# Performance work log

Hardware: AMD Instinct MI355X
Metric: run time of the kernel (lower is better)

## Reference

```python
import jax, jax.numpy as jnp
import numpy as np

B, C, D, H, W = 4, 1, 4, 768, 768
STRICT_MAXIMA_BONUS = 10.0

_c = slice(1, -1)
_l = slice(0, -2)
_r = slice(2, None)


def _pad_rep(x):
    # replicate-pad the three spatial dims by 1 (matches F.pad mode='replicate')
    return jnp.pad(x, ((0, 0), (0, 0), (1, 1), (1, 1), (1, 1)), mode='edge')


def _grads(x):
    """kornia spatial_gradient3d(mode='diff') order 1 and 2, incl. the D-axis
    kernel flip kornia applies before conv3d (negates the ys/xs cross terms)."""
    p = _pad_rep(x)
    gx = 0.5 * (p[:, :, _c, _c, _r] - p[:, :, _c, _c, _l])
    gy = 0.5 * (p[:, :, _c, _r, _c] - p[:, :, _c, _l, _c])
    gs = 0.5 * (p[:, :, _r, _c, _c] - p[:, :, _l, _c, _c])
    dxx = p[:, :, _c, _c, _r] - 2.0 * x + p[:, :, _c, _c, _l]
    dyy = p[:, :, _c, _r, _c] - 2.0 * x + p[:, :, _c, _l, _c]
    dss = p[:, :, _r, _c, _c] - 2.0 * x + p[:, :, _l, _c, _c]
    # cross terms, scaled by 0.25 as in conv_quad_interp3d
    dxy = 0.25 * (p[:, :, _c, _r, _r] - p[:, :, _c, _r, _l] - p[:, :, _c, _l, _r] + p[:, :, _c, _l, _l])
    dys = -0.25 * (p[:, :, _r, _r, _c] - p[:, :, _r, _l, _c] - p[:, :, _l, _r, _c] + p[:, :, _l, _l, _c])
    dxs = -0.25 * (p[:, :, _r, _c, _r] - p[:, :, _r, _c, _l] - p[:, :, _l, _c, _r] + p[:, :, _l, _c, _l])
    return gx, gy, gs, dxx, dyy, dss, dxy, dys, dxs


def _nms3d_strict(x):
    """kornia nms3d 3x3x3 mask: x strictly greater than all 26 neighbours
    (replicate padded) AND x > 0 (the zeroed-center kernel channel)."""
    p = _pad_rep(x)
    sl = [_l, _c, _r]
    m = jnp.zeros_like(x)  # center channel of the NMS kernel is zeroed
    for a in range(3):
        for b in range(3):
            for c3 in range(3):
                if a == 1 and b == 1 and c3 == 1:
                    continue
                m = jnp.maximum(m, p[:, :, sl[a], sl[b], sl[c3]])
    return x > m


def _conv_quad_interp3d(x, strict_maxima_bonus):
    gx, gy, gs, dxx, dyy, dss, dxy, dys, dxs = _grads(x)
    nms_mask = _nms3d_strict(x)
    # per-voxel symmetric 3x3 Cramer solve H s = g
    cf00 = dyy * dss - dys * dys
    cf01 = dxy * dss - dys * dxs
    cf02 = dxy * dys - dyy * dxs
    det = dxx * cf00 - dxy * cf01 + dxs * cf02
    solved = jnp.abs(det) > 0.0
    safe_det = jnp.where(solved, det, jnp.ones_like(det))
    r0, r1, r2 = gx, gy, gs
    sx = (r0 * cf00 - dxy * (r1 * dss - dys * r2) + dxs * (r1 * dys - dyy * r2)) / safe_det
    sy = (dxx * (r1 * dss - dys * r2) - r0 * cf01 + dxs * (dxy * r2 - r1 * dxs)) / safe_det
    ss = (dxx * (dyy * r2 - r1 * dys) - dxy * (dxy * r2 - r1 * dxs) + r0 * cf02) / safe_det
    valid = nms_mask & solved
    # x_solved only where NMS & non-singular; dx = -x_solved
    dx_x = jnp.where(valid, -sx, 0.0)
    dx_y = jnp.where(valid, -sy, 0.0)
    dx_s = jnp.where(valid, -ss, 0.0)
    # reject offsets with |component| > 0.7
    big = jnp.maximum(jnp.maximum(jnp.abs(dx_x), jnp.abs(dx_y)), jnp.abs(dx_s)) > 0.7
    dx_x = jnp.where(big, 0.0, dx_x)
    dx_y = jnp.where(big, 0.0, dx_y)
    dx_s = jnp.where(big, 0.0, dx_s)
    # dy = 0.5 * b^T dx
    dy = 0.5 * (gx * dx_x + gy * dx_y + gs * dx_s)
    y_max = x + dy
    if strict_maxima_bonus > 0:
        y_max = y_max + strict_maxima_bonus * valid.astype(x.dtype)
    # coords: channel order (d, x, y) as in kornia create_meshgrid3d + channel swap
    b_, c_, d_, h_, w_ = x.shape
    zz = jnp.arange(d_, dtype=x.dtype).reshape(1, 1, d_, 1, 1)
    xxg = jnp.arange(w_, dtype=x.dtype).reshape(1, 1, 1, 1, w_)
    yyg = jnp.arange(h_, dtype=x.dtype).reshape(1, 1, 1, h_, 1)
    coords_max = jnp.stack([zz + dx_s, xxg + dx_x, yyg + dx_y], axis=2)  # (B,C,3,D,H,W)
    return coords_max, y_max


def setup_inputs() -> dict:
    key = jax.random.key(0)
    x = jax.random.normal(key, (B, C, D, H, W), dtype=jnp.float32)
    return {"x": x}


def reference(x):
    return _conv_quad_interp3d(x, STRICT_MAXIMA_BONUS)
```

## Files before the change

### kernel.cpp

```cpp
#include <hip/hip_runtime.h>

namespace {
constexpr int Bn = 4, Dn = 4, Hn = 768, Wn = 768;
constexpr int HWc = Hn * Wn;
constexpr size_t DHWc = (size_t)Dn * HWc;
constexpr float BONUS = 10.0f;
}

__global__ __launch_bounds__(192) void cqi3d(const float* __restrict__ x,
                                             float* __restrict__ coords,
                                             float* __restrict__ ymax) {
#pragma clang fp contract(off)
    int id = blockIdx.x;
    id = (id & 7) * ((Hn * Bn) >> 3) + (id >> 3);
    const int h = id % Hn;
    const int b = id / Hn;
    const int t = threadIdx.x;
    const int w0 = t << 2;

    const float* base = x + (size_t)b * DHWc;
    float* cb = coords + (size_t)b * 3 * DHWc;
    float* yb = ymax + (size_t)b * DHWc;

    const float4 cz0 = make_float4(0.f, 0.f, 0.f, 0.f);
    const float4 cz3 = make_float4(3.f, 3.f, 3.f, 3.f);
    const float4 cx  = make_float4((float)w0, (float)(w0 + 1), (float)(w0 + 2), (float)(w0 + 3));
    const float4 cy  = make_float4((float)h, (float)h, (float)h, (float)h);

    if (h == 0 || h == Hn - 1) {
#pragma unroll
        for (int d = 0; d < 4; ++d) {
            const size_t sp = (size_t)d * HWc + (size_t)h * Wn + (size_t)w0;
            const float4 q = *reinterpret_cast<const float4*>(base + sp);
            *reinterpret_cast<float4*>(cb + sp)            = make_float4((float)d, (float)d, (float)d, (float)d);
            *reinterpret_cast<float4*>(cb + DHWc + sp)     = cx;
            *reinterpret_cast<float4*>(cb + 2 * DHWc + sp) = cy;
            *reinterpret_cast<float4*>(yb + sp)            = q;
        }
        return;
    }

    const int wl = (w0 == 0) ? 0 : w0 - 1;
    const int wr = (w0 + 4 < Wn) ? w0 + 4 : Wn - 1;
    const int hz[3] = {h - 1, h, h + 1};

    float v[3][4][6];
#pragma unroll
    for (int a = 0; a < 3; ++a) {
#pragma unroll
        for (int dd = 0; dd < 4; ++dd) {
            const float* ph = base + (size_t)dd * HWc + (size_t)hz[a] * Wn;
            const float4 q = *reinterpret_cast<const float4*>(ph + w0);
            v[a][dd][0] = ph[wl];
            v[a][dd][1] = q.x;
            v[a][dd][2] = q.y;
            v[a][dd][3] = q.z;
            v[a][dd][4] = q.w;
            v[a][dd][5] = ph[wr];
        }
    }

    {
        const size_t sp0 = (size_t)h * Wn + (size_t)w0;
        *reinterpret_cast<float4*>(cb + sp0)            = cz0;
        *reinterpret_cast<float4*>(cb + DHWc + sp0)     = cx;
        *reinterpret_cast<float4*>(cb + 2 * DHWc + sp0) = cy;
        *reinterpret_cast<float4*>(yb + sp0)            = make_float4(v[1][0][1], v[1][0][2], v[1][0][3], v[1][0][4]);
        const size_t sp3 = 3 * (size_t)HWc + sp0;
        *reinterpret_cast<float4*>(cb + sp3)            = cz3;
        *reinterpret_cast<float4*>(cb + DHWc + sp3)     = cx;
        *reinterpret_cast<float4*>(cb + 2 * DHWc + sp3) = cy;
        *reinterpret_cast<float4*>(yb + sp3)            = make_float4(v[1][3][1], v[1][3][2], v[1][3][3], v[1][3][4]);
    }

#pragma unroll
    for (int d = 1; d <= 2; ++d) {
        const int s0 = d - 1;
        const int s2 = d + 1;
        float colNC[6], cmax[6];
#pragma unroll
        for (int c = 0; c < 6; ++c) {
            float m = v[0][s0][c];
            m = fmaxf(m, v[1][s0][c]);
            m = fmaxf(m, v[2][s0][c]);
            m = fmaxf(m, v[0][d][c]);
            m = fmaxf(m, v[2][d][c]);
            m = fmaxf(m, v[0][s2][c]);
            m = fmaxf(m, v[1][s2][c]);
            m = fmaxf(m, v[2][s2][c]);
            colNC[c] = m;
            cmax[c] = fmaxf(m, v[1][d][c]);
        }

        float outz[4], outx[4], outy[4], outv[4];
#pragma unroll
        for (int j = 0; j < 4; ++j) {
            const int cc = j + 1;
            const float xc = v[1][d][cc];
            const float m = fmaxf(fmaxf(cmax[cc - 1], cmax[cc + 1]), fmaxf(colNC[cc], 0.0f));
            const bool nms = xc > m;

            const float gx  = 0.5f * (v[1][d][cc + 1] - v[1][d][cc - 1]);
            const float gy  = 0.5f * (v[2][d][cc] - v[0][d][cc]);
            const float gs  = 0.5f * (v[1][s2][cc] - v[1][s0][cc]);
            const float dxx = v[1][d][cc + 1] - 2.0f * xc + v[1][d][cc - 1];
            const float dyy = v[2][d][cc] - 2.0f * xc + v[0][d][cc];
            const float dss = v[1][s2][cc] - 2.0f * xc + v[1][s0][cc];
            const float dxy =  0.25f * (v[2][d][cc + 1] - v[2][d][cc - 1] - v[0][d][cc + 1] + v[0][d][cc - 1]);
            const float dys = -0.25f * (v[2][s2][cc] - v[0][s2][cc] - v[2][s0][cc] + v[0][s0][cc]);
            const float dxs = -0.25f * (v[1][s2][cc + 1] - v[1][s2][cc - 1] - v[1][s0][cc + 1] + v[1][s0][cc - 1]);

            const float cf00 = dyy * dss - dys * dys;
            const float cf01 = dxy * dss - dys * dxs;
            const float cf02 = dxy * dys - dyy * dxs;
            const float det  = dxx * cf00 - dxy * cf01 + dxs * cf02;
            const bool solved = fabsf(det) > 0.0f;
            const float sd = solved ? det : 1.0f;

            const float t0 = gy * dss - dys * gs;
            const float sx = (gx * cf00 - dxy * t0 + dxs * (gy * dys - dyy * gs)) / sd;
            const float sy = (dxx * t0 - gx * cf01 + dxs * (dxy * gs - gy * dxs)) / sd;
            const float ss = (dxx * (dyy * gs - gy * dys) - dxy * (dxy * gs - gy * dxs) + gx * cf02) / sd;

            const bool valid = nms && solved;
            float dxv = valid ? -sx : 0.0f;
            float dyv = valid ? -sy : 0.0f;
            float dsv = valid ? -ss : 0.0f;
            const float mx = fmaxf(fmaxf(fabsf(dxv), fabsf(dyv)), fabsf(dsv));
            if (mx > 0.7f) { dxv = 0.0f; dyv = 0.0f; dsv = 0.0f; }

            const float dy_ = 0.5f * (gx * dxv + gy * dyv + gs * dsv);
            float y = xc + dy_;
            if (valid) y += BONUS;

            outz[j] = (float)d + dsv;
            outx[j] = (float)(w0 + j) + dxv;
            outy[j] = (float)h + dyv;
            outv[j] = y;
        }

        const size_t sp = (size_t)d * HWc + (size_t)h * Wn + (size_t)w0;
        *reinterpret_cast<float4*>(cb + sp)            = make_float4(outz[0], outz[1], outz[2], outz[3]);
        *reinterpret_cast<float4*>(cb + DHWc + sp)     = make_float4(outx[0], outx[1], outx[2], outx[3]);
        *reinterpret_cast<float4*>(cb + 2 * DHWc + sp) = make_float4(outy[0], outy[1], outy[2], outy[3]);
        *reinterpret_cast<float4*>(yb + sp)            = make_float4(outv[0], outv[1], outv[2], outv[3]);
    }
}

extern "C" void kernel_launch(void* const* d_in, const int* in_sizes, int n_in,
                              void* d_out, int out_size, void* d_ws, size_t ws_size,
                              hipStream_t stream) {
    const float* x = (const float*)d_in[0];
    float* out = (float*)d_out;
    float* coords = out;
    float* ymaxp  = out + (size_t)Bn * 3 * DHWc;
    cqi3d<<<dim3(Hn * Bn), dim3(192, 1, 1), 0, stream>>>(x, coords, ymaxp);
}
```

Before: 34.68 us.

## Process 4-row H strips per block with rolling row register buffer

```diff
diff --git a/kernel.cpp b/kernel.cpp
--- a/kernel.cpp
+++ b/kernel.cpp
@@ -5,72 +5,60 @@
 constexpr int HWc = Hn * Wn;
 constexpr size_t DHWc = (size_t)Dn * HWc;
 constexpr float BONUS = 10.0f;
+constexpr int HSTRIP = 4;
+constexpr int NSTRIP = Hn / HSTRIP;
+constexpr int NBLK = Bn * NSTRIP;
 }
 
-__global__ __launch_bounds__(192) void cqi3d(const float* __restrict__ x,
-                                             float* __restrict__ coords,
-                                             float* __restrict__ ymax) {
+__device__ __forceinline__ void load_row(float (&dst)[4][6], const float* __restrict__ base,
+                                         int row, int w0, int wl, int wr) {
+#pragma unroll
+    for (int dd = 0; dd < 4; ++dd) {
+        const float* ph = base + (size_t)dd * HWc + (size_t)row * Wn;
+        const float4 q = *reinterpret_cast<const float4*>(ph + w0);
+        dst[dd][0] = ph[wl];
+        dst[dd][1] = q.x;
+        dst[dd][2] = q.y;
+        dst[dd][3] = q.z;
+        dst[dd][4] = q.w;
+        dst[dd][5] = ph[wr];
+    }
+}
+
+__device__ __forceinline__ void row_trivial(const float (&vc)[4][6],
+                                            float* __restrict__ cb, float* __restrict__ yb,
+                                            int h, int w0) {
+    const float4 cx = make_float4((float)w0, (float)(w0 + 1), (float)(w0 + 2), (float)(w0 + 3));
+    const float4 cy = make_float4((float)h, (float)h, (float)h, (float)h);
+#pragma unroll
+    for (int d = 0; d < 4; ++d) {
+        const size_t sp = (size_t)d * HWc + (size_t)h * Wn + (size_t)w0;
+        *reinterpret_cast<float4*>(cb + sp)            = make_float4((float)d, (float)d, (float)d, (float)d);
+        *reinterpret_cast<float4*>(cb + DHWc + sp)     = cx;
+        *reinterpret_cast<float4*>(cb + 2 * DHWc + sp) = cy;
+        *reinterpret_cast<float4*>(yb + sp)            = make_float4(vc[d][1], vc[d][2], vc[d][3], vc[d][4]);
+    }
+}
+
+__device__ __forceinline__ void compute_row(const float (&vm)[4][6], const float (&vc)[4][6],
+                                            const float (&vp)[4][6],
+                                            float* __restrict__ cb, float* __restrict__ yb,
+                                            int h, int w0) {
 #pragma clang fp contract(off)
-    int id = blockIdx.x;
-    id = (id & 7) * ((Hn * Bn) >> 3) + (id >> 3);
-    const int h = id % Hn;
-    const int b = id / Hn;
-    const int t = threadIdx.x;
-    const int w0 = t << 2;
-
-    const float* base = x + (size_t)b * DHWc;
-    float* cb = coords + (size_t)b * 3 * DHWc;
-    float* yb = ymax + (size_t)b * DHWc;
-
-    const float4 cz0 = make_float4(0.f, 0.f, 0.f, 0.f);
-    const float4 cz3 = make_float4(3.f, 3.f, 3.f, 3.f);
-    const float4 cx  = make_float4((float)w0, (float)(w0 + 1), (float)(w0 + 2), (float)(w0 + 3));
-    const float4 cy  = make_float4((float)h, (float)h, (float)h, (float)h);
-
-    if (h == 0 || h == Hn - 1) {
-#pragma unroll
-        for (int d = 0; d < 4; ++d) {
-            const size_t sp = (size_t)d * HWc + (size_t)h * Wn + (size_t)w0;
-            const float4 q = *reinterpret_cast<const float4*>(base + sp);
-            *reinterpret_cast<float4*>(cb + sp)            = make_float4((float)d, (float)d, (float)d, (float)d);
-            *reinterpret_cast<float4*>(cb + DHWc + sp)     = cx;
-            *reinterpret_cast<float4*>(cb + 2 * DHWc + sp) = cy;
-            *reinterpret_cast<float4*>(yb + sp)            = q;
-        }
-        return;
-    }
-
-    const int wl = (w0 == 0) ? 0 : w0 - 1;
-    const int wr = (w0 + 4 < Wn) ? w0 + 4 : Wn - 1;
-    const int hz[3] = {h - 1, h, h + 1};
-
-    float v[3][4][6];
-#pragma unroll
-    for (int a = 0; a < 3; ++a) {
-#pragma unroll
-        for (int dd = 0; dd < 4; ++dd) {
-            const float* ph = base + (size_t)dd * HWc + (size_t)hz[a] * Wn;
-            const float4 q = *reinterpret_cast<const float4*>(ph + w0);
-            v[a][dd][0] = ph[wl];
-            v[a][dd][1] = q.x;
-            v[a][dd][2] = q.y;
-            v[a][dd][3] = q.z;
-            v[a][dd][4] = q.w;
-            v[a][dd][5] = ph[wr];
-        }
-    }
+    const float4 cx = make_float4((float)w0, (float)(w0 + 1), (float)(w0 + 2), (float)(w0 + 3));
+    const float4 cy = make_float4((float)h, (float)h, (float)h, (float)h);
 
     {
         const size_t sp0 = (size_t)h * Wn + (size_t)w0;
-        *reinterpret_cast<float4*>(cb + sp0)            = cz0;
+        *reinterpret_cast<float4*>(cb + sp0)            = make_float4(0.f, 0.f, 0.f, 0.f);
         *reinterpret_cast<float4*>(cb + DHWc + sp0)     = cx;
         *reinterpret_cast<float4*>(cb + 2 * DHWc + sp0) = cy;
-        *reinterpret_cast<float4*>(yb + sp0)            = make_float4(v[1][0][1], v[1][0][2], v[1][0][3], v[1][0][4]);
+        *reinterpret_cast<float4*>(yb + sp0)            = make_float4(vc[0][1], vc[0][2], vc[0][3], vc[0][4]);
         const size_t sp3 = 3 * (size_t)HWc + sp0;
-        *reinterpret_cast<float4*>(cb + sp3)            = cz3;
+        *reinterpret_cast<float4*>(cb + sp3)            = make_float4(3.f, 3.f, 3.f, 3.f);
         *reinterpret_cast<float4*>(cb + DHWc + sp3)     = cx;
         *reinterpret_cast<float4*>(cb + 2 * DHWc + sp3) = cy;
-        *reinterpret_cast<float4*>(yb + sp3)            = make_float4(v[1][3][1], v[1][3][2], v[1][3][3], v[1][3][4]);
+        *reinterpret_cast<float4*>(yb + sp3)            = make_float4(vc[3][1], vc[3][2], vc[3][3], vc[3][4]);
     }
 
 #pragma unroll
@@ -80,35 +68,35 @@
         float colNC[6], cmax[6];
 #pragma unroll
         for (int c = 0; c < 6; ++c) {
-            float m = v[0][s0][c];
-            m = fmaxf(m, v[1][s0][c]);
-            m = fmaxf(m, v[2][s0][c]);
-            m = fmaxf(m, v[0][d][c]);
-            m = fmaxf(m, v[2][d][c]);
-            m = fmaxf(m, v[0][s2][c]);
-            m = fmaxf(m, v[1][s2][c]);
-            m = fmaxf(m, v[2][s2][c]);
+            float m = vm[s0][c];
+            m = fmaxf(m, vc[s0][c]);
+            m = fmaxf(m, vp[s0][c]);
+            m = fmaxf(m, vm[d][c]);
+            m = fmaxf(m, vp[d][c]);
+            m = fmaxf(m, vm[s2][c]);
+            m = fmaxf(m, vc[s2][c]);
+            m = fmaxf(m, vp[s2][c]);
             colNC[c] = m;
-            cmax[c] = fmaxf(m, v[1][d][c]);
+            cmax[c] = fmaxf(m, vc[d][c]);
         }
 
         float outz[4], outx[4], outy[4], outv[4];
 #pragma unroll
         for (int j = 0; j < 4; ++j) {
             const int cc = j + 1;
-            const float xc = v[1][d][cc];
+            const float xc = vc[d][cc];
             const float m = fmaxf(fmaxf(cmax[cc - 1], cmax[cc + 1]), fmaxf(colNC[cc], 0.0f));
             const bool nms = xc > m;
 
-            const float gx  = 0.5f * (v[1][d][cc + 1] - v[1][d][cc - 1]);
-            const float gy  = 0.5f * (v[2][d][cc] - v[0][d][cc]);
-            const float gs  = 0.5f * (v[1][s2][cc] - v[1][s0][cc]);
-            const float dxx = v[1][d][cc + 1] - 2.0f * xc + v[1][d][cc - 1];
-            const float dyy = v[2][d][cc] - 2.0f * xc + v[0][d][cc];
-            const float dss = v[1][s2][cc] - 2.0f * xc + v[1][s0][cc];
-            const float dxy =  0.25f * (v[2][d][cc + 1] - v[2][d][cc - 1] - v[0][d][cc + 1] + v[0][d][cc - 1]);
-            const float dys = -0.25f * (v[2][s2][cc] - v[0][s2][cc] - v[2][s0][cc] + v[0][s0][cc]);
-            const float dxs = -0.25f * (v[1][s2][cc + 1] - v[1][s2][cc - 1] - v[1][s0][cc + 1] + v[1][s0][cc - 1]);
+            const float gx  = 0.5f * (vc[d][cc + 1] - vc[d][cc - 1]);
+            const float gy  = 0.5f * (vp[d][cc] - vm[d][cc]);
+            const float gs  = 0.5f * (vc[s2][cc] - vc[s0][cc]);
+            const float dxx = vc[d][cc + 1] - 2.0f * xc + vc[d][cc - 1];
+            const float dyy = vp[d][cc] - 2.0f * xc + vm[d][cc];
+            const float dss = vc[s2][cc] - 2.0f * xc + vc[s0][cc];
+            const float dxy =  0.25f * (vp[d][cc + 1] - vp[d][cc - 1] - vm[d][cc + 1] + vm[d][cc - 1]);
+            const float dys = -0.25f * (vp[s2][cc] - vm[s2][cc] - vp[s0][cc] + vm[s0][cc]);
+            const float dxs = -0.25f * (vc[s2][cc + 1] - vc[s2][cc - 1] - vc[s0][cc + 1] + vc[s0][cc - 1]);
 
             const float cf00 = dyy * dss - dys * dys;
             const float cf01 = dxy * dss - dys * dxs;
@@ -147,6 +135,53 @@
     }
 }
 
+__global__ __launch_bounds__(192) void cqi3d(const float* __restrict__ x,
+                                             float* __restrict__ coords,
+                                             float* __restrict__ ymax) {
+#pragma clang fp contract(off)
+    int id = blockIdx.x;
+    id = (id & 7) * (NBLK >> 3) + (id >> 3);
+    const int strip = id % NSTRIP;
+    const int b = id / NSTRIP;
+    const int h0 = strip * HSTRIP;
+    const int t = threadIdx.x;
+    const int w0 = t << 2;
+
+    const float* base = x + (size_t)b * DHWc;
+    float* cb = coords + (size_t)b * 3 * DHWc;
+    float* yb = ymax + (size_t)b * DHWc;
+    const int wl = (w0 == 0) ? 0 : w0 - 1;
+    const int wr = (w0 + 4 < Wn) ? w0 + 4 : Wn - 1;
+
+    if (strip == 0 || strip == NSTRIP - 1) {
+        for (int i = 0; i < HSTRIP; ++i) {
+            const int hh = h0 + i;
+            float vm[4][6], vc[4][6], vp[4][6];
+            load_row(vc, base, hh, w0, wl, wr);
+            if (hh == 0 || hh == Hn - 1) {
+                row_trivial(vc, cb, yb, hh, w0);
+                continue;
+            }
+            load_row(vm, base, hh - 1, w0, wl, wr);
+            load_row(vp, base, hh + 1, w0, wl, wr);
+            compute_row(vm, vc, vp, cb, yb, hh, w0);
+        }
+        return;
+    }
+
+    float v[4][4][6];
+    load_row(v[0], base, h0 - 1, w0, wl, wr);
+    load_row(v[1], base, h0,     w0, wl, wr);
+    load_row(v[2], base, h0 + 1, w0, wl, wr);
+#pragma unroll
+    for (int i = 0; i < HSTRIP; ++i) {
+        const int hh = h0 + i;
+        if (i < HSTRIP - 1)
+            load_row(v[(i + 3) & 3], base, hh + 2, w0, wl, wr);
+        compute_row(v[i & 3], v[(i + 1) & 3], v[(i + 2) & 3], cb, yb, hh, w0);
+    }
+}
+
 extern "C" void kernel_launch(void* const* d_in, const int* in_sizes, int n_in,
                               void* d_out, int out_size, void* d_ws, size_t ws_size,
                               hipStream_t stream) {
@@ -154,5 +189,5 @@
     float* out = (float*)d_out;
     float* coords = out;
     float* ymaxp  = out + (size_t)Bn * 3 * DHWc;
-    cqi3d<<<dim3(Hn * Bn), dim3(192, 1, 1), 0, stream>>>(x, coords, ymaxp);
+    cqi3d<<<dim3(NBLK), dim3(192, 1, 1), 0, stream>>>(x, coords, ymaxp);
 }
```

New measurement: 40.96 us. 1.18x slower.
